# Kernel optimization log

Measured on AMD Instinct MI355X. Metric: run time of the kernel, lower is better.

The kernel has to match this reference:

```python
import jax, jax.numpy as jnp
import numpy as np

N_NODES = 100000
K_NEIGH = 16
C = 128
B = 1


def setup_inputs() -> dict:
    key = jax.random.key(0)
    k1, k2, k3, k4, k5, k6 = jax.random.split(key, 6)
    inp = jax.random.normal(k1, (B, C, N_NODES), dtype=jnp.float32)
    adj = jax.random.randint(k2, (N_NODES, K_NEIGH), 0, N_NODES)
    w1 = jax.random.normal(k3, (C, C), dtype=jnp.float32) * 0.05
    b1 = jax.random.normal(k4, (C,), dtype=jnp.float32) * 0.05
    w2 = jax.random.normal(k5, (C, C), dtype=jnp.float32) * 0.05
    b2 = jax.random.normal(k6, (C,), dtype=jnp.float32) * 0.05
    return {"input": inp, "adj": adj, "w1": w1, "b1": b1, "w2": w2, "b2": b2}


def reference(input, adj, w1, b1, w2, b2):
    # fc1: 1x1 conv == channel-mixing matmul. input: [B, C, N]
    state_in = jnp.einsum('oc,bcn->bon', w1, input) + b1[None, :, None]
    # gather neighbor features: [B, C, N, K], mean over neighbors -> [B, C, N]
    neigh = input[:, :, adj]            # [B, C, N, K]
    agg = neigh.mean(axis=3)            # [B, C, N]
    fwd = jnp.einsum('oc,bcn->bon', w2, agg) + b2[None, :, None]
    return state_in + fwd
```

## Files before the change

### kernel.cpp

```cpp
#include <hip/hip_runtime.h>
#include <stdint.h>

#define N_NODES 100000
#define CH 128
#define K_NEIGH 16
#define TN 32
#define XS_STRIDE 68
#define PS 132

#define PSWZ(n, o) ((n) * PS + ((o) ^ ((((n) >> 3) & 3) << 3)))


typedef short bf8v __attribute__((ext_vector_type(8)));
typedef float f32x4 __attribute__((ext_vector_type(4)));

__device__ __forceinline__ uint32_t pack_bf16x2(float a, float b) {
    union { float f; uint32_t u; } ua, ub;
    ua.f = a; ub.f = b;
    const uint32_t ra = (ua.u + 0x7fffu + ((ua.u >> 16) & 1u)) >> 16;
    const uint32_t rb = (ub.u + 0x7fffu + ((ub.u >> 16) & 1u)) >> 16;
    return ra | (rb << 16);
}
__device__ __forceinline__ uint16_t bf16_rne(float f) {
    union { float f; uint32_t u; } c; c.f = f;
    return (uint16_t)((c.u + 0x7fffu + ((c.u >> 16) & 1u)) >> 16);
}
__device__ __forceinline__ float bf16_tof(uint16_t h) {
    union { uint32_t u; float f; } c; c.u = ((uint32_t)h) << 16; return c.f;
}
__device__ __forceinline__ float bf16_lo(uint32_t u) {
    union { uint32_t u; float f; } c; c.u = u << 16; return c.f;
}
__device__ __forceinline__ float bf16_hi(uint32_t u) {
    union { uint32_t u; float f; } c; c.u = u & 0xffff0000u; return c.f;
}

__global__ void k_wcvt(const float* __restrict__ W,
                       uint16_t* __restrict__ Wh, uint16_t* __restrict__ Wl) {
    const int i = blockIdx.x * 256 + threadIdx.x;
    if (i < CH * CH) {
        const float f = W[i];
        const uint16_t h = bf16_rne(f);
        Wh[i] = h;
        Wl[i] = bf16_rne(f - bf16_tof(h));
    }
}

__global__ __launch_bounds__(256, 2) void k_dual(
    const float*    __restrict__ X,
    const uint16_t* __restrict__ W1h,
    const uint16_t* __restrict__ W1l,
    const uint16_t* __restrict__ W2h,
    const uint16_t* __restrict__ W2l,
    const float*    __restrict__ B1,
    const float*    __restrict__ B2,
    uint16_t*       __restrict__ Yt,
    float*          __restrict__ Out)
{
    __shared__ __align__(16) uint16_t XsH[64 * 128];
    __shared__ __align__(16) uint16_t XsL[64 * 128];

    const int t  = threadIdx.x;
    const int n0 = blockIdx.x * 64;
    const int V  = (N_NODES - n0 < 64) ? (N_NODES - n0) : 64;

    for (int it = 0; it < 8; ++it) {
        const int idx = t + it * 256;
        const int nq = idx & 15, c = idx >> 4;
        float4 v = make_float4(0.f, 0.f, 0.f, 0.f);
        if (nq * 4 < V)
            v = *(const float4*)&X[(size_t)c * N_NODES + n0 + nq * 4];
        const float vv0 = v.x, vv1 = v.y, vv2 = v.z, vv3 = v.w;
#pragma unroll
        for (int s = 0; s < 4; ++s) {
            const float f = (s == 0) ? vv0 : (s == 1) ? vv1 : (s == 2) ? vv2 : vv3;
            const int n = nq * 4 + s;
            const int byi = (n << 8) + (((c * 2)) ^ ((n & 7) << 4));
            const uint16_t h = bf16_rne(f);
            XsH[byi >> 1] = h;
            XsL[byi >> 1] = bf16_rne(f - bf16_tof(h));
        }
    }
    __syncthreads();

    const int l = t & 63;
    const int w = t >> 6;
    const int ar = l & 15;
    const int ac = (l >> 4) * 8;

    f32x4 d1[2][4], d2[2][4];
#pragma unroll
    for (int ot = 0; ot < 2; ++ot)
#pragma unroll
        for (int nt = 0; nt < 4; ++nt) {
            d1[ot][nt] = (f32x4){0.f, 0.f, 0.f, 0.f};
            d2[ot][nt] = (f32x4){0.f, 0.f, 0.f, 0.f};
        }

#pragma unroll
    for (int ks = 0; ks < 4; ++ks) {
        bf8v a1h[2], a1l[2], a2h[2], a2l[2];
#pragma unroll
        for (int ot = 0; ot < 2; ++ot) {
            const size_t off = (size_t)(w * 32 + ot * 16 + ar) * CH + ks * 32 + ac;
            a1h[ot] = *(const bf8v*)&W1h[off];
            a1l[ot] = *(const bf8v*)&W1l[off];
            a2h[ot] = *(const bf8v*)&W2h[off];
            a2l[ot] = *(const bf8v*)&W2l[off];
        }
#pragma unroll
        for (int nt = 0; nt < 4; ++nt) {
            const int n  = nt * 16 + (l & 15);
            const int byi = (n << 8) + ((ks * 64 + ((l >> 4) * 16)) ^ ((n & 7) << 4));
            const bf8v bh = *(const bf8v*)((const char*)XsH + byi);
            const bf8v bl = *(const bf8v*)((const char*)XsL + byi);
#pragma unroll
            for (int ot = 0; ot < 2; ++ot) {
                d1[ot][nt] = __builtin_amdgcn_mfma_f32_16x16x32_bf16(
                    a1h[ot], bh, d1[ot][nt], 0, 0, 0);
                d1[ot][nt] = __builtin_amdgcn_mfma_f32_16x16x32_bf16(
                    a1l[ot], bh, d1[ot][nt], 0, 0, 0);
                d1[ot][nt] = __builtin_amdgcn_mfma_f32_16x16x32_bf16(
                    a1h[ot], bl, d1[ot][nt], 0, 0, 0);
                d2[ot][nt] = __builtin_amdgcn_mfma_f32_16x16x32_bf16(
                    a2h[ot], bh, d2[ot][nt], 0, 0, 0);
                d2[ot][nt] = __builtin_amdgcn_mfma_f32_16x16x32_bf16(
                    a2l[ot], bh, d2[ot][nt], 0, 0, 0);
            }
        }
    }

#pragma unroll
    for (int ot = 0; ot < 2; ++ot) {
        const int ob = w * 32 + ot * 16 + (l >> 4) * 4;
        const float b0 = B1[ob + 0] + B2[ob + 0];
        const float b1 = B1[ob + 1] + B2[ob + 1];
        const float b2 = B1[ob + 2] + B2[ob + 2];
        const float b3 = B1[ob + 3] + B2[ob + 3];
#pragma unroll
        for (int nt = 0; nt < 4; ++nt) {
            const int n = nt * 16 + (l & 15);
            if (n < V) {
                float* op = Out + (size_t)ob * N_NODES + n0 + n;
                op[0]                   = d1[ot][nt][0] + b0;
                op[(size_t)N_NODES]     = d1[ot][nt][1] + b1;
                op[(size_t)N_NODES * 2] = d1[ot][nt][2] + b2;
                op[(size_t)N_NODES * 3] = d1[ot][nt][3] + b3;
            }
        }
    }

#pragma unroll
    for (int ot = 0; ot < 2; ++ot)
#pragma unroll
        for (int nt = 0; nt < 4; ++nt) {
            const int n = nt * 16 + (l & 15);
            if (n < V) {
                const int o4 = w * 32 + ot * 16 + (l >> 4) * 4;
                uint2 pv;
                pv.x = pack_bf16x2(d2[ot][nt][0], d2[ot][nt][1]);
                pv.y = pack_bf16x2(d2[ot][nt][2], d2[ot][nt][3]);
                *(uint2*)&Yt[(size_t)(n0 + n) * CH + o4] = pv;
            }
        }
}

__global__ __launch_bounds__(256, 8) void k_gather(
    const int*      __restrict__ adj,
    const uint16_t* __restrict__ Yt,
    float*          __restrict__ Out)
{
    __shared__ __align__(16) float P[TN * PS];
    __shared__ __align__(16) int adjS[TN * K_NEIGH];

    const int t  = threadIdx.x;
    const int n0 = blockIdx.x * TN;

    if (t < 128)
        *(int4*)&adjS[t * 4] = *(const int4*)&adj[(size_t)n0 * K_NEIGH + t * 4];
    __syncthreads();

    {
        const int l4 = (t & 31) * 4;
        const int g  = t >> 5;
        for (int itp = 0; itp < 4; ++itp) {
            const int n = itp * 8 + g;
            int js[K_NEIGH];
#pragma unroll
            for (int k = 0; k < K_NEIGH; ++k) js[k] = adjS[n * K_NEIGH + k];
            float4 a0 = make_float4(0.f, 0.f, 0.f, 0.f);
            float4 a1 = make_float4(0.f, 0.f, 0.f, 0.f);
#pragma unroll
            for (int k = 0; k < K_NEIGH; k += 2) {
                const uint2 v0 = *(const uint2*)&Yt[(size_t)js[k]     * CH + l4];
                const uint2 v1 = *(const uint2*)&Yt[(size_t)js[k + 1] * CH + l4];
                a0.x += bf16_lo(v0.x); a0.y += bf16_hi(v0.x);
                a0.z += bf16_lo(v0.y); a0.w += bf16_hi(v0.y);
                a1.x += bf16_lo(v1.x); a1.y += bf16_hi(v1.x);
                a1.z += bf16_lo(v1.y); a1.w += bf16_hi(v1.y);
            }
            float4 s;
            s.x = (a0.x + a1.x) * 0.0625f;
            s.y = (a0.y + a1.y) * 0.0625f;
            s.z = (a0.z + a1.z) * 0.0625f;
            s.w = (a0.w + a1.w) * 0.0625f;
            *(float4*)&P[PSWZ(n, l4)] = s;
        }
    }
    __syncthreads();

    for (int it = 0; it < 4; ++it) {
        const int idx = t + it * 256;
        const int o = idx >> 3, nq = idx & 7;
        float* op = Out + (size_t)o * N_NODES + n0 + nq * 4;
        float4 cur = *(const float4*)op;
        cur.x += P[PSWZ(nq * 4 + 0, o)];
        cur.y += P[PSWZ(nq * 4 + 1, o)];
        cur.z += P[PSWZ(nq * 4 + 2, o)];
        cur.w += P[PSWZ(nq * 4 + 3, o)];
        *(float4*)op = cur;
    }
}

__global__ __launch_bounds__(256, 2) void k_fused_legacy(
    const float* __restrict__ X,
    const int*   __restrict__ adj,
    const float* __restrict__ W1,
    const float* __restrict__ B1,
    const float* __restrict__ W2,
    const float* __restrict__ B2,
    float*       __restrict__ Out)
{
    __shared__ __align__(16) float Xs[CH * XS_STRIDE];
    __shared__ __align__(16) float As[CH * XS_STRIDE];
    __shared__ int adjS[64 * K_NEIGH];

    const int t  = threadIdx.x;
    const int n0 = blockIdx.x * 64;
    const int V  = (N_NODES - n0 < 64) ? (N_NODES - n0) : 64;

    {
        const int base  = n0 * K_NEIGH;
        const int valid = V * K_NEIGH;
        for (int idx = t; idx < 64 * K_NEIGH; idx += 256)
            adjS[idx] = (idx < valid) ? adj[base + idx] : 0;
    }
    for (int it = 0; it < 32; ++it) {
        const int idx = t + it * 256;
        const int n = idx & 63, c = idx >> 6;
        Xs[c * XS_STRIDE + n] =
            (n < V) ? X[(size_t)c * N_NODES + n0 + n] : 0.0f;
    }
    __syncthreads();

    {
        const int n_l = t & 63, q = t >> 6;
        int js[K_NEIGH];
#pragma unroll
        for (int k = 0; k < K_NEIGH; ++k) js[k] = adjS[n_l * K_NEIGH + k];
        if (n_l < V) {
            for (int cc = 0; cc < 32; ++cc) {
                const int c = q * 32 + cc;
                const float* xc = X + (size_t)c * N_NODES;
                float s = 0.0f;
#pragma unroll
                for (int k = 0; k < K_NEIGH; ++k) s += xc[js[k]];
                As[c * XS_STRIDE + n_l] = s * 0.0625f;
            }
        } else {
            for (int cc = 0; cc < 32; ++cc)
                As[(q * 32 + cc) * XS_STRIDE + n_l] = 0.0f;
        }
    }
    __syncthreads();

    const int ng = t & 7, og = t >> 3;
    float acc[4][8];
#pragma unroll
    for (int i = 0; i < 4; ++i)
#pragma unroll
        for (int j = 0; j < 8; ++j) acc[i][j] = 0.0f;

    const float* w1p = W1 + (og * 4) * CH;
    const float* w2p = W2 + (og * 4) * CH;
    for (int c = 0; c < CH; ++c) {
        float xv[8], av[8], w1v[4], w2v[4];
        *(float4*)&xv[0] = *(const float4*)&Xs[c * XS_STRIDE + ng * 8];
        *(float4*)&xv[4] = *(const float4*)&Xs[c * XS_STRIDE + ng * 8 + 4];
        *(float4*)&av[0] = *(const float4*)&As[c * XS_STRIDE + ng * 8];
        *(float4*)&av[4] = *(const float4*)&As[c * XS_STRIDE + ng * 8 + 4];
#pragma unroll
        for (int i = 0; i < 4; ++i) {
            w1v[i] = w1p[i * CH + c];
            w2v[i] = w2p[i * CH + c];
        }
#pragma unroll
        for (int i = 0; i < 4; ++i)
#pragma unroll
            for (int j = 0; j < 8; ++j)
                acc[i][j] += w1v[i] * xv[j] + w2v[i] * av[j];
    }

    __syncthreads();
    float* Zt = Xs;
#pragma unroll
    for (int i = 0; i < 4; ++i) {
        *(float4*)&Zt[(og * 4 + i) * XS_STRIDE + ng * 8]     = *(float4*)&acc[i][0];
        *(float4*)&Zt[(og * 4 + i) * XS_STRIDE + ng * 8 + 4] = *(float4*)&acc[i][4];
    }
    __syncthreads();
    for (int it = 0; it < 32; ++it) {
        const int idx = t + it * 256;
        const int n = idx & 63, o = idx >> 6;
        if (n < V) {
            Out[(size_t)o * N_NODES + n0 + n] =
                Zt[o * XS_STRIDE + n] + B1[o] + B2[o];
        }
    }
}

extern "C" void kernel_launch(void* const* d_in, const int* in_sizes, int n_in,
                              void* d_out, int out_size, void* d_ws, size_t ws_size,
                              hipStream_t stream) {
    const float* X   = (const float*)d_in[0];
    const int*   adj = (const int*)d_in[1];
    const float* W1  = (const float*)d_in[2];
    const float* B1  = (const float*)d_in[3];
    const float* W2  = (const float*)d_in[4];
    const float* B2  = (const float*)d_in[5];
    float* Out = (float*)d_out;

    const size_t yt_elems = (size_t)N_NODES * CH;
    const size_t w_elems  = (size_t)CH * CH;
    const size_t need = (yt_elems + 4 * w_elems) * sizeof(uint16_t);

    if (ws_size >= need) {
        uint16_t* Yt  = (uint16_t*)d_ws;
        uint16_t* W1h = Yt + yt_elems;
        uint16_t* W1l = W1h + w_elems;
        uint16_t* W2h = W1l + w_elems;
        uint16_t* W2l = W2h + w_elems;
        const int wcb = (CH * CH + 255) / 256;
        k_wcvt<<<wcb, 256, 0, stream>>>(W1, W1h, W1l);
        k_wcvt<<<wcb, 256, 0, stream>>>(W2, W2h, W2l);
        const int nb1 = (N_NODES + 63) / 64;
        k_dual<<<nb1, 256, 0, stream>>>(X, W1h, W1l, W2h, W2l, B1, B2, Yt, Out);
        const int nb2 = N_NODES / TN;
        k_gather<<<nb2, 256, 0, stream>>>(adj, Yt, Out);
    } else {
        const int nblocks = (N_NODES + 63) / 64;
        k_fused_legacy<<<nblocks, 256, 0, stream>>>(X, adj, W1, B1, W2, B2, Out);
    }
}
```

Baseline: 236.8 us.

## Merge weight conversions, batch X loads, widen gather loads to 16 bytes

New measurement: 269.8 us. +14.0%, slower.

```diff
diff --git a/kernel.cpp b/kernel.cpp
--- a/kernel.cpp
+++ b/kernel.cpp
@@ -35,14 +35,21 @@
     union { uint32_t u; float f; } c; c.u = u & 0xffff0000u; return c.f;
 }
 
-__global__ void k_wcvt(const float* __restrict__ W,
-                       uint16_t* __restrict__ Wh, uint16_t* __restrict__ Wl) {
+__global__ void k_wcvt2(const float* __restrict__ W1, const float* __restrict__ W2,
+                        uint16_t* __restrict__ W1h, uint16_t* __restrict__ W1l,
+                        uint16_t* __restrict__ W2h, uint16_t* __restrict__ W2l) {
     const int i = blockIdx.x * 256 + threadIdx.x;
     if (i < CH * CH) {
-        const float f = W[i];
+        const float f = W1[i];
         const uint16_t h = bf16_rne(f);
-        Wh[i] = h;
-        Wl[i] = bf16_rne(f - bf16_tof(h));
+        W1h[i] = h;
+        W1l[i] = bf16_rne(f - bf16_tof(h));
+    } else if (i < 2 * CH * CH) {
+        const int j = i - CH * CH;
+        const float f = W2[j];
+        const uint16_t h = bf16_rne(f);
+        W2h[j] = h;
+        W2l[j] = bf16_rne(f - bf16_tof(h));
     }
 }
 
@@ -64,13 +71,20 @@
     const int n0 = blockIdx.x * 64;
     const int V  = (N_NODES - n0 < 64) ? (N_NODES - n0) : 64;
 
+    float4 v[8];
+#pragma unroll
     for (int it = 0; it < 8; ++it) {
         const int idx = t + it * 256;
         const int nq = idx & 15, c = idx >> 4;
-        float4 v = make_float4(0.f, 0.f, 0.f, 0.f);
+        v[it] = make_float4(0.f, 0.f, 0.f, 0.f);
         if (nq * 4 < V)
-            v = *(const float4*)&X[(size_t)c * N_NODES + n0 + nq * 4];
-        const float vv0 = v.x, vv1 = v.y, vv2 = v.z, vv3 = v.w;
+            v[it] = *(const float4*)&X[(size_t)c * N_NODES + n0 + nq * 4];
+    }
+#pragma unroll
+    for (int it = 0; it < 8; ++it) {
+        const int idx = t + it * 256;
+        const int nq = idx & 15, c = idx >> 4;
+        const float vv0 = v[it].x, vv1 = v[it].y, vv2 = v[it].z, vv3 = v[it].w;
 #pragma unroll
         for (int s = 0; s < 4; ++s) {
             const float f = (s == 0) ? vv0 : (s == 1) ? vv1 : (s == 2) ? vv2 : vv3;
@@ -97,7 +111,7 @@
             d2[ot][nt] = (f32x4){0.f, 0.f, 0.f, 0.f};
         }
 
-#pragma unroll
+#pragma unroll 2
     for (int ks = 0; ks < 4; ++ks) {
         bf8v a1h[2], a1l[2], a2h[2], a2l[2];
 #pragma unroll
@@ -181,30 +195,41 @@
     __syncthreads();
 
     {
-        const int l4 = (t & 31) * 4;
-        const int g  = t >> 5;
-        for (int itp = 0; itp < 4; ++itp) {
-            const int n = itp * 8 + g;
+        const int q = t & 15;
+        const int g = t >> 4;
+#pragma unroll
+        for (int r = 0; r < 2; ++r) {
+            const int n = r * 16 + g;
             int js[K_NEIGH];
 #pragma unroll
             for (int k = 0; k < K_NEIGH; ++k) js[k] = adjS[n * K_NEIGH + k];
-            float4 a0 = make_float4(0.f, 0.f, 0.f, 0.f);
-            float4 a1 = make_float4(0.f, 0.f, 0.f, 0.f);
+            float c0[8], c1[8];
+#pragma unroll
+            for (int j = 0; j < 8; ++j) { c0[j] = 0.f; c1[j] = 0.f; }
 #pragma unroll
             for (int k = 0; k < K_NEIGH; k += 2) {
-                const uint2 v0 = *(const uint2*)&Yt[(size_t)js[k]     * CH + l4];
-                const uint2 v1 = *(const uint2*)&Yt[(size_t)js[k + 1] * CH + l4];
-                a0.x += bf16_lo(v0.x); a0.y += bf16_hi(v0.x);
-                a0.z += bf16_lo(v0.y); a0.w += bf16_hi(v0.y);
-                a1.x += bf16_lo(v1.x); a1.y += bf16_hi(v1.x);
-                a1.z += bf16_lo(v1.y); a1.w += bf16_hi(v1.y);
-            }
-            float4 s;
-            s.x = (a0.x + a1.x) * 0.0625f;
-            s.y = (a0.y + a1.y) * 0.0625f;
-            s.z = (a0.z + a1.z) * 0.0625f;
-            s.w = (a0.w + a1.w) * 0.0625f;
-            *(float4*)&P[PSWZ(n, l4)] = s;
+                const uint4 A = *(const uint4*)&Yt[(size_t)js[k]     * CH + q * 8];
+                const uint4 B = *(const uint4*)&Yt[(size_t)js[k + 1] * CH + q * 8];
+                c0[0] += bf16_lo(A.x); c0[1] += bf16_hi(A.x);
+                c0[2] += bf16_lo(A.y); c0[3] += bf16_hi(A.y);
+                c0[4] += bf16_lo(A.z); c0[5] += bf16_hi(A.z);
+                c0[6] += bf16_lo(A.w); c0[7] += bf16_hi(A.w);
+                c1[0] += bf16_lo(B.x); c1[1] += bf16_hi(B.x);
+                c1[2] += bf16_lo(B.y); c1[3] += bf16_hi(B.y);
+                c1[4] += bf16_lo(B.z); c1[5] += bf16_hi(B.z);
+                c1[6] += bf16_lo(B.w); c1[7] += bf16_hi(B.w);
+            }
+            float4 s0, s1;
+            s0.x = (c0[0] + c1[0]) * 0.0625f;
+            s0.y = (c0[1] + c1[1]) * 0.0625f;
+            s0.z = (c0[2] + c1[2]) * 0.0625f;
+            s0.w = (c0[3] + c1[3]) * 0.0625f;
+            s1.x = (c0[4] + c1[4]) * 0.0625f;
+            s1.y = (c0[5] + c1[5]) * 0.0625f;
+            s1.z = (c0[6] + c1[6]) * 0.0625f;
+            s1.w = (c0[7] + c1[7]) * 0.0625f;
+            *(float4*)&P[PSWZ(n, q * 8)]     = s0;
+            *(float4*)&P[PSWZ(n, q * 8 + 4)] = s1;
         }
     }
     __syncthreads();
@@ -340,9 +365,8 @@
         uint16_t* W1l = W1h + w_elems;
         uint16_t* W2h = W1l + w_elems;
         uint16_t* W2l = W2h + w_elems;
-        const int wcb = (CH * CH + 255) / 256;
-        k_wcvt<<<wcb, 256, 0, stream>>>(W1, W1h, W1l);
-        k_wcvt<<<wcb, 256, 0, stream>>>(W2, W2h, W2l);
+        k_wcvt2<<<(2 * CH * CH + 255) / 256, 256, 0, stream>>>(
+            W1, W2, W1h, W1l, W2h, W2l);
         const int nb1 = (N_NODES + 63) / 64;
         k_dual<<<nb1, 256, 0, stream>>>(X, W1h, W1l, W2h, W2l, B1, B2, Yt, Out);
         const int nb2 = N_NODES / TN;
```
